# Performance work log

Measured on AMD Instinct MI355X. Metric: run time of the kernel, lower is better.

Reference implementation:

```python
import math
import jax, jax.numpy as jnp
import numpy as np

HEAD_DIM = 128
NUM_HEADS = 16
NUM_KV_HEADS = 4
CAUSAL = True


def rotate_half(x):
    x1 = x[..., : x.shape[-1] // 2]
    x2 = x[..., x.shape[-1] // 2 :]
    return jnp.concatenate([-x2, x1], axis=-1)


def setup_inputs() -> dict:
    key = jax.random.key(0)
    k1, k2, k3, k4, k5 = jax.random.split(key, 5)
    B, S, H = 2, 2048, 2048
    total_heads = NUM_HEADS + 2 * NUM_KV_HEADS  # 24
    hidden_states = jax.random.normal(k1, (B, S, H), dtype=jnp.float32)
    cos = jax.random.normal(k2, (S, HEAD_DIM), dtype=jnp.float32)
    sin = jax.random.normal(k3, (S, HEAD_DIM), dtype=jnp.float32)
    # eqx.nn.Linear weight layout: [out_features, in_features], y = W @ x
    w_qkv = jax.random.normal(k4, (total_heads * HEAD_DIM, H), dtype=jnp.float32) / math.sqrt(H)
    w_o = jax.random.normal(k5, (H, NUM_HEADS * HEAD_DIM), dtype=jnp.float32) / math.sqrt(NUM_HEADS * HEAD_DIM)
    return {"hidden_states": hidden_states, "cos": cos, "sin": sin, "w_qkv": w_qkv, "w_o": w_o}


def reference(hidden_states, cos, sin, w_qkv, w_o):
    B, S, _ = hidden_states.shape
    # fused QKV projection: [B,S,total_heads,head_dim]
    qkv = jnp.einsum("bsh,oh->bso", hidden_states, w_qkv).reshape(B, S, -1, HEAD_DIM)
    q = qkv[:, :, :NUM_HEADS]
    k = qkv[:, :, NUM_HEADS : NUM_HEADS + NUM_KV_HEADS]
    v = qkv[:, :, NUM_HEADS + NUM_KV_HEADS :]
    # RoPE: cos/sin [S,head_dim] -> broadcast [S,1,head_dim] over heads
    c = cos[..., None, :]
    s_ = sin[..., None, :]
    q = q * c + rotate_half(q) * s_
    k = k * c + rotate_half(k) * s_
    # GQA: repeat K/V across query-head groups
    rep = NUM_HEADS // NUM_KV_HEADS
    k = jnp.repeat(k, rep, axis=2)
    v = jnp.repeat(v, rep, axis=2)
    scale = 1.0 / math.sqrt(HEAD_DIM)
    scores = jnp.einsum("bshd,bthd->bhst", q, k) * scale  # [B,H,S,S]
    if CAUSAL:
        mask = jnp.tril(jnp.ones((S, S), dtype=bool))[None, None]
        scores = jnp.where(mask, scores, jnp.float32(-1e10))
    attn = jax.nn.softmax(scores, axis=-1)
    out = jnp.einsum("bhst,bthd->bshd", attn, v).reshape(B, S, -1)
    return jnp.einsum("bsd,od->bso", out, w_o)
```

## Files before the change

kernel.cpp:

```cpp
#include <hip/hip_runtime.h>
#include <hip/hip_bf16.h>
#include <stdint.h>

typedef __hip_bfloat16 bf16;
typedef __attribute__((ext_vector_type(8))) __bf16 bf16x8;
typedef __attribute__((ext_vector_type(4))) float f32x4;
typedef __attribute__((ext_vector_type(16))) float f32x16;
typedef __attribute__((ext_vector_type(4))) unsigned int u32x4;

#define QSCALE_LOG2E (0.08838834764831845f * 1.4426950408889634f)

__device__ __forceinline__ float fast_exp2(float x) {
#if __has_builtin(__builtin_amdgcn_exp2f)
  return __builtin_amdgcn_exp2f(x);
#else
  return exp2f(x);
#endif
}

__device__ __forceinline__ void gload_lds16(const void* g, void* l) {
  __builtin_amdgcn_global_load_lds(
      (__attribute__((address_space(1))) void*)(uintptr_t)g,
      (__attribute__((address_space(3))) void*)(uint32_t)(uintptr_t)l,
      16, 0, 0);
}

__global__ void cast_f32_to_bf16(const float* __restrict__ in,
                                 bf16* __restrict__ out, int n) {
  const int n4 = n >> 2;
  const int stride = gridDim.x * blockDim.x;
  for (int i = blockIdx.x * blockDim.x + threadIdx.x; i < n4; i += stride) {
    float4 v = reinterpret_cast<const float4*>(in)[i];
    bf16 tmp[4];
    tmp[0] = __float2bfloat16(v.x);
    tmp[1] = __float2bfloat16(v.y);
    tmp[2] = __float2bfloat16(v.z);
    tmp[3] = __float2bfloat16(v.w);
    reinterpret_cast<uint2*>(out)[i] = *reinterpret_cast<uint2*>(tmp);
  }
}

__device__ __forceinline__ void store_c(float v, bf16* p) { *p = __float2bfloat16(v); }
__device__ __forceinline__ void store_c(float v, float* p) { *p = v; }

__device__ __forceinline__ bf16x8 rd_swz(const bf16* base, int row, int ks, int hi) {
  const int byte = row * 128 + ((ks * 64 + hi * 16) ^ ((row & 7) << 4));
  return *reinterpret_cast<const bf16x8*>((const char*)base + byte);
}

__device__ __forceinline__ void stage_part(const bf16* __restrict__ g, int K,
                                           int kt, bf16* ldsBase, int part,
                                           int tid) {
  const int ga = part * 512 + tid;
  const int r = ga >> 3;
  const int gl = ga & 7;
  const int col = kt * 64 + ((gl ^ (r & 7)) << 3);
  gload_lds16(g + (size_t)r * K + col, (char*)ldsBase + ga * 16);
}

#define DS_A(QR)                                                              \
  _Pragma("unroll") for (int m = 0; m < 4; ++m)                               \
  _Pragma("unroll") for (int ks = 0; ks < 2; ++ks)                            \
      af[m][ks] = rd_swz(Acur, wm * 128 + (QR) * 64 + m * 16 + lr, ks, hi);

#define DS_B0()                                                               \
  _Pragma("unroll") for (int n = 0; n < NQ0; ++n)                             \
  _Pragma("unroll") for (int ks = 0; ks < 2; ++ks)                            \
      bf0[n][ks] = rd_swz(Bcur, wn * WN + n * 16 + lr, ks, hi);

#define DS_B1()                                                               \
  _Pragma("unroll") for (int n = 0; n < NQ1; ++n)                             \
  _Pragma("unroll") for (int ks = 0; ks < 2; ++ks)                            \
      bf1[n][ks] = rd_swz(Bcur, wn * WN + (NQ0 + n) * 16 + lr, ks, hi);

#define MFMA_Q0(QR)                                                           \
  __builtin_amdgcn_s_setprio(1);                                             \
  _Pragma("unroll") for (int ks = 0; ks < 2; ++ks)                            \
  _Pragma("unroll") for (int m = 0; m < 4; ++m)                               \
  _Pragma("unroll") for (int n = 0; n < NQ0; ++n)                             \
      acc[(QR) * 4 + m][n] = __builtin_amdgcn_mfma_f32_16x16x32_bf16(         \
          af[m][ks], bf0[n][ks], acc[(QR) * 4 + m][n], 0, 0, 0);              \
  __builtin_amdgcn_s_setprio(0);

#define MFMA_Q1(QR)                                                           \
  __builtin_amdgcn_s_setprio(1);                                             \
  _Pragma("unroll") for (int ks = 0; ks < 2; ++ks)                            \
  _Pragma("unroll") for (int m = 0; m < 4; ++m)                               \
  _Pragma("unroll") for (int n = 0; n < NQ1; ++n)                             \
      acc[(QR) * 4 + m][NQ0 + n] = __builtin_amdgcn_mfma_f32_16x16x32_bf16(   \
          af[m][ks], bf1[n][ks], acc[(QR) * 4 + m][NQ0 + n], 0, 0, 0);        \
  __builtin_amdgcn_s_setprio(0);

#define PHASE_SYNC_PRE()                                \
  __builtin_amdgcn_s_barrier();                         \
  asm volatile("s_waitcnt lgkmcnt(0)" ::: "memory");    \
  __builtin_amdgcn_sched_barrier(0);

#define PHASE_END() __builtin_amdgcn_s_barrier();

#define VMCNT_LB()                                                            \
  if constexpr (LB == 2) asm volatile("s_waitcnt vmcnt(2)" ::: "memory");     \
  else if constexpr (LB == 3) asm volatile("s_waitcnt vmcnt(3)" ::: "memory");\
  else asm volatile("s_waitcnt vmcnt(4)" ::: "memory");

template <int BN, typename OutT>
__global__ __launch_bounds__(512, 2) void gemm256(const bf16* __restrict__ A,
                                                  const bf16* __restrict__ B,
                                                  OutT* __restrict__ C,
                                                  int M, int N, int K, int NBX) {
  constexpr int NFRAG = BN / 64;
  constexpr int NQ0 = (NFRAG + 1) / 2;
  constexpr int NQ1 = NFRAG - NQ0;
  constexpr int WN = BN / 4;
  constexpr int LB = BN / 64;
  constexpr int LB0 = (LB + 1) / 2;
  constexpr int LB1 = LB - LB0;

  extern __shared__ bf16 sm[];
  bf16* A0 = sm;
  bf16* A1 = sm + 16384;
  bf16* B0 = sm + 32768;
  bf16* B1 = B0 + BN * 64;

  const int tid = threadIdx.x;
  const int lane = tid & 63;
  const int w = tid >> 6;
  const int wm = w >> 2;
  const int wn = w & 3;
  const int lr = lane & 15;
  const int hi = lane >> 4;

  const int nwg = gridDim.x;
  const int cpx = nwg >> 3;
  const int bid = blockIdx.x;
  const int wg = (bid & 7) * cpx + (bid >> 3);
  const int bx = wg % NBX;
  const int by = wg / NBX;
  const int row0 = by * 256;
  const int col0 = bx * BN;

  const bf16* Ag = A + (size_t)row0 * K;
  const bf16* Bg = B + (size_t)col0 * K;

#pragma unroll
  for (int p = 0; p < 4; ++p) stage_part(Ag, K, 0, A0, p, tid);
#pragma unroll
  for (int p = 0; p < LB; ++p) stage_part(Bg, K, 0, B0, p, tid);
#pragma unroll
  for (int p = 0; p < LB; ++p) stage_part(Bg, K, 1, B1, p, tid);
  VMCNT_LB();
  __builtin_amdgcn_s_barrier();

  f32x4 acc[8][NFRAG] = {};
  bf16x8 af[4][2], bf0[NQ0][2], bf1[NQ1 ? NQ1 : 1][2];

  const int iters = K >> 7;
  for (int i = 0; i < iters; ++i) {
    const bool g2 = (i + 1 < iters);
    const int t1 = 2 * i + 1, t2 = 2 * i + 2, t3 = 2 * i + 3;
    {
      const bf16* Acur = A0;
      const bf16* Bcur = B0;
      DS_A(0); DS_B0();
      stage_part(Ag, K, t1, A1, 0, tid);
      stage_part(Ag, K, t1, A1, 1, tid);
      PHASE_SYNC_PRE(); MFMA_Q0(0); PHASE_END();
      DS_B1();
      stage_part(Ag, K, t1, A1, 2, tid);
      stage_part(Ag, K, t1, A1, 3, tid);
      PHASE_SYNC_PRE(); MFMA_Q1(0); PHASE_END();
      DS_A(1);
      if (g2) {
#pragma unroll
        for (int p = 0; p < LB0; ++p) stage_part(Bg, K, t2, B0, p, tid);
      }
      PHASE_SYNC_PRE(); MFMA_Q0(1); PHASE_END();
      if (g2) {
#pragma unroll
        for (int p = 0; p < LB1; ++p) stage_part(Bg, K, t2, B0, LB0 + p, tid);
        VMCNT_LB();
      } else {
        asm volatile("s_waitcnt vmcnt(0)" ::: "memory");
      }
      PHASE_SYNC_PRE(); MFMA_Q1(1); PHASE_END();
    }
    {
      const bf16* Acur = A1;
      const bf16* Bcur = B1;
      DS_A(0); DS_B0();
      if (g2) {
        stage_part(Ag, K, t2, A0, 0, tid);
        stage_part(Ag, K, t2, A0, 1, tid);
      }
      PHASE_SYNC_PRE(); MFMA_Q0(0); PHASE_END();
      DS_B1();
      if (g2) {
        stage_part(Ag, K, t2, A0, 2, tid);
        stage_part(Ag, K, t2, A0, 3, tid);
      }
      PHASE_SYNC_PRE(); MFMA_Q1(0); PHASE_END();
      DS_A(1);
      if (g2) {
#pragma unroll
        for (int p = 0; p < LB0; ++p) stage_part(Bg, K, t3, B1, p, tid);
      }
      PHASE_SYNC_PRE(); MFMA_Q0(1); PHASE_END();
      if (g2) {
#pragma unroll
        for (int p = 0; p < LB1; ++p) stage_part(Bg, K, t3, B1, LB0 + p, tid);
        VMCNT_LB();
      } else {
        asm volatile("s_waitcnt vmcnt(0)" ::: "memory");
      }
      PHASE_SYNC_PRE(); MFMA_Q1(1); PHASE_END();
    }
  }

#pragma unroll
  for (int mi = 0; mi < 8; ++mi)
#pragma unroll
    for (int ni = 0; ni < NFRAG; ++ni)
#pragma unroll
      for (int j = 0; j < 4; ++j) {
        const int r = row0 + wm * 128 + mi * 16 + hi * 4 + j;
        const int cc = col0 + wn * WN + ni * 16 + lr;
        store_c(acc[mi][ni][j], &C[(size_t)r * N + cc]);
      }
}

__global__ void rope_scatter(const bf16* __restrict__ qkv,
                             const float* __restrict__ cs,
                             const float* __restrict__ sn,
                             bf16* __restrict__ Q, bf16* __restrict__ Kd) {
  const int tok = blockIdx.x;
  const int b = tok >> 11;
  const int s = tok & 2047;
  const bf16* row = qkv + (size_t)tok * 3072;
  for (int idx = threadIdx.x; idx < 1280; idx += blockDim.x) {
    const int head = idx >> 6;
    const int j = idx & 63;
    float x1 = __bfloat162float(row[head * 128 + j]);
    float x2 = __bfloat162float(row[head * 128 + j + 64]);
    const float c1 = cs[s * 128 + j];
    const float c2 = cs[s * 128 + j + 64];
    const float s1 = sn[s * 128 + j];
    const float s2 = sn[s * 128 + j + 64];
    float y1 = x1 * c1 - x2 * s1;
    float y2 = x2 * c2 + x1 * s2;
    bf16* dst;
    if (head < 16) {
      y1 *= QSCALE_LOG2E;
      y2 *= QSCALE_LOG2E;
      dst = Q + ((size_t)(b * 16 + head) * 2048 + s) * 128;
    } else {
      dst = Kd + ((size_t)(b * 4 + head - 16) * 2048 + s) * 128;
    }
    dst[j] = __float2bfloat16(y1);
    dst[j + 64] = __float2bfloat16(y2);
  }
}

__global__ __launch_bounds__(256) void vtrans(const bf16* __restrict__ qkv,
                                              bf16* __restrict__ Vt) {
  __shared__ bf16 tile[64 * 136];
  const int bid = blockIdx.x;
  const int stile = bid & 31;
  const int hv = (bid >> 5) & 3;
  const int b = bid >> 7;
  const int tid = threadIdx.x;
  const int tok0 = stile * 64;
  const bf16* src = qkv + (size_t)(b * 2048 + tok0) * 3072 + 2560 + hv * 128;
#pragma unroll
  for (int i = 0; i < 4; ++i) {
    const int c = tid + i * 256;
    const int r = c >> 4;
    const int off = (c & 15) * 8;
    uint4 d = *reinterpret_cast<const uint4*>(src + (size_t)r * 3072 + off);
    *reinterpret_cast<uint4*>(&tile[r * 136 + off]) = d;
  }
  __syncthreads();
  bf16* dst = Vt + ((size_t)(b * 4 + hv) * 128) * 2048 + tok0;
#pragma unroll
  for (int i = 0; i < 4; ++i) {
    const int o = tid + i * 256;
    const int d = o >> 3;
    const int s0 = (o & 7) * 8;
    bf16 vals[8];
#pragma unroll
    for (int j = 0; j < 8; ++j) vals[j] = tile[(s0 + j) * 136 + d];
    *reinterpret_cast<uint4*>(dst + (size_t)d * 2048 + s0) =
        *reinterpret_cast<const uint4*>(vals);
  }
}

__device__ __forceinline__ void stage_k(const bf16* __restrict__ Kb, int k0,
                                        bf16* dst, int w, int lane) {
#pragma unroll
  for (int i = 0; i < 4; ++i) {
    const int L16 = i * 256 + w * 64 + lane;
    const int row = L16 >> 4;
    const int colb = (L16 & 15) * 16;
    const int src = colb ^ ((row & 7) << 4);
    gload_lds16(Kb + (size_t)(k0 + row) * 128 + (src >> 1),
                (char*)dst + (i * 256 + w * 64) * 16);
  }
}

__device__ __forceinline__ void stage_v(const bf16* __restrict__ Vtb, int k0,
                                        bf16* dst, int w, int lane) {
#pragma unroll
  for (int i = 0; i < 4; ++i) {
    const int L16 = i * 256 + w * 64 + lane;
    const int row = L16 >> 3;
    const int colb = (L16 & 7) * 16;
    const int src = colb ^ ((row & 7) << 4);
    gload_lds16(Vtb + (size_t)row * 2048 + k0 + (src >> 1),
                (char*)dst + (i * 256 + w * 64) * 16);
  }
}

__device__ __forceinline__ bf16x8 lds_read_swz(const bf16* base, int row,
                                               int colElem, int rowBytes) {
  const int byte = row * rowBytes + (((colElem * 2) ^ ((row & 7) << 4)));
  return *reinterpret_cast<const bf16x8*>((const char*)base + byte);
}

__global__ __launch_bounds__(256, 2) void attn_fwd(const bf16* __restrict__ Qg,
                                                   const bf16* __restrict__ Kg,
                                                   const bf16* __restrict__ Vtg,
                                                   bf16* __restrict__ Og) {
  __shared__ bf16 Ks[2][64 * 128];
  __shared__ bf16 Vs[2][128 * 64];

  const int tid = threadIdx.x;
  const int lane = tid & 63;
  const int w = tid >> 6;
  const int bid = blockIdx.x;
  int qt, bh;
  if (bid < 256) { qt = bid & 15; bh = bid >> 4; }
  else           { qt = 15 - (bid & 15); bh = 16 + ((bid - 256) >> 4); }
  const int b = bh >> 4;
  const int h = bh & 15;
  const int kvh = h >> 2;
  const int q31 = lane & 31;
  const int hw = lane >> 5;

  const bf16* Qb = Qg + ((size_t)(b * 16 + h) * 2048) * 128;
  const bf16* Kb = Kg + ((size_t)(b * 4 + kvh) * 2048) * 128;
  const bf16* Vtb = Vtg + ((size_t)(b * 4 + kvh) * 128) * 2048;

  const int qw = qt * 128 + w * 32;

  bf16x8 qf[8];
#pragma unroll
  for (int db = 0; db < 8; ++db)
    qf[db] = *reinterpret_cast<const bf16x8*>(Qb + (size_t)(qw + q31) * 128 +
                                              db * 16 + hw * 8);

  f32x16 acc[4] = {};
  float mrow = -1e30f;
  float lsum = 0.f;

  const int nt = 2 * qt + 2;

  stage_k(Kb, 0, &Ks[0][0], w, lane);
  stage_v(Vtb, 0, &Vs[0][0], w, lane);

  for (int t = 0; t < nt; ++t) {
    const int cur = t & 1;
    if (t + 1 < nt) {
      stage_k(Kb, (t + 1) * 64, &Ks[cur ^ 1][0], w, lane);
      stage_v(Vtb, (t + 1) * 64, &Vs[cur ^ 1][0], w, lane);
      asm volatile("s_waitcnt vmcnt(8)" ::: "memory");
    } else {
      asm volatile("s_waitcnt vmcnt(0)" ::: "memory");
    }
    __builtin_amdgcn_s_barrier();
    __builtin_amdgcn_sched_barrier(0);

    const int k0 = t * 64;
    const bool active = (k0 <= qw + 31);
    if (active) {
      const bf16* Kt = &Ks[cur][0];
      const bf16* Vtl = &Vs[cur][0];

      f32x16 sacc[2] = {};
#pragma unroll
      for (int kb = 0; kb < 2; ++kb)
#pragma unroll
        for (int db = 0; db < 8; ++db) {
          bf16x8 kf = lds_read_swz(Kt, kb * 32 + q31, db * 16 + hw * 8, 256);
          sacc[kb] = __builtin_amdgcn_mfma_f32_32x32x16_bf16(kf, qf[db],
                                                             sacc[kb], 0, 0, 0);
        }

      float p[2][16];
#pragma unroll
      for (int kb = 0; kb < 2; ++kb)
#pragma unroll
        for (int r = 0; r < 16; ++r) p[kb][r] = sacc[kb][r];

      if (k0 + 63 > qw) {
        const int qg = qw + q31;
#pragma unroll
        for (int kb = 0; kb < 2; ++kb)
#pragma unroll
          for (int r = 0; r < 16; ++r) {
            const int k = k0 + kb * 32 + (r & 3) + 8 * (r >> 2) + 4 * hw;
            if (k > qg) p[kb][r] = -1e30f;
          }
      }

      float mt = p[0][0];
#pragma unroll
      for (int r = 1; r < 16; ++r) mt = fmaxf(mt, p[0][r]);
#pragma unroll
      for (int r = 0; r < 16; ++r) mt = fmaxf(mt, p[1][r]);
      mt = fmaxf(mt, __shfl_xor(mt, 32));

      if (__any(mt > mrow + 11.5f)) {
        const float mnew = fmaxf(mrow, mt);
        const float alpha = fast_exp2(mrow - mnew);
        mrow = mnew;
        lsum *= alpha;
        float areg[16];
#pragma unroll
        for (int r = 0; r < 16; ++r) {
          const int qloc = (r & 3) + 8 * (r >> 2) + 4 * hw;
          areg[r] = __shfl(alpha, qloc + (lane & 32));
        }
#pragma unroll
        for (int db = 0; db < 4; ++db)
#pragma unroll
          for (int r = 0; r < 16; ++r) acc[db][r] *= areg[r];
      }

      float rs = 0.f;
#pragma unroll
      for (int kb = 0; kb < 2; ++kb)
#pragma unroll
        for (int r = 0; r < 16; ++r) {
          const float pe = fast_exp2(p[kb][r] - mrow);
          p[kb][r] = pe;
          rs += pe;
        }
      rs += __shfl_xor(rs, 32);
      lsum += rs;

      unsigned int pk[2][8];
#pragma unroll
      for (int kb = 0; kb < 2; ++kb)
#pragma unroll
        for (int i = 0; i < 8; ++i)
          asm("v_cvt_pk_bf16_f32 %0, %1, %2"
              : "=v"(pk[kb][i])
              : "v"(p[kb][2 * i]), "v"(p[kb][2 * i + 1]));

#pragma unroll
      for (int kb16 = 0; kb16 < 4; ++kb16) {
        const int kb = kb16 >> 1;
        const int j0 = (kb16 & 1) * 4;
        unsigned int a0 = pk[kb][j0 + 0], b0 = pk[kb][j0 + 2];
        unsigned int a1 = pk[kb][j0 + 1], b1 = pk[kb][j0 + 3];
        asm volatile("v_permlane32_swap_b32 %0, %1" : "+v"(a0), "+v"(b0));
        asm volatile("v_permlane32_swap_b32 %0, %1" : "+v"(a1), "+v"(b1));
        u32x4 afu;
        afu.x = a0; afu.y = a1; afu.z = b0; afu.w = b1;
        bf16x8 pa;
        __builtin_memcpy(&pa, &afu, 16);
#pragma unroll
        for (int db = 0; db < 4; ++db) {
          bf16x8 vf = lds_read_swz(Vtl, db * 32 + q31, kb16 * 16 + hw * 8, 128);
          acc[db] = __builtin_amdgcn_mfma_f32_32x32x16_bf16(pa, vf,
                                                            acc[db], 0, 0, 0);
        }
      }
    }

    __builtin_amdgcn_sched_barrier(0);
    __builtin_amdgcn_s_barrier();
  }

  const float inv = 1.0f / lsum;
  float invq[16];
#pragma unroll
  for (int r = 0; r < 16; ++r) {
    const int qloc = (r & 3) + 8 * (r >> 2) + 4 * hw;
    invq[r] = __shfl(inv, qloc + (lane & 32));
  }
#pragma unroll
  for (int db = 0; db < 4; ++db)
#pragma unroll
    for (int r = 0; r < 16; ++r) {
      const int qg = qw + (r & 3) + 8 * (r >> 2) + 4 * hw;
      const int dg = db * 32 + q31;
      Og[((size_t)(b * 2048 + qg)) * 2048 + h * 128 + dg] =
          __float2bfloat16(acc[db][r] * invq[r]);
    }
}

extern "C" void kernel_launch(void* const* d_in, const int* in_sizes, int n_in,
                              void* d_out, int out_size, void* d_ws,
                              size_t ws_size, hipStream_t stream) {
  const float* hidden = (const float*)d_in[0];
  const float* cs = (const float*)d_in[1];
  const float* sn = (const float*)d_in[2];
  const float* wqkv = (const float*)d_in[3];
  const float* wo = (const float*)d_in[4];
  float* out = (float*)d_out;

  bf16* p = (bf16*)d_ws;
  bf16* hid_b = p;   p += 8388608;
  bf16* wqkv_b = p;  p += 6291456;
  bf16* wo_b = p;    p += 4194304;
  bf16* qkv = p;     p += 12582912;
  bf16* Qs = p;      p += 8388608;
  bf16* Ksc = p;     p += 2097152;
  bf16* Vt = p;      p += 2097152;

  (void)hipFuncSetAttribute((const void*)gemm256<192, bf16>,
                            hipFuncAttributeMaxDynamicSharedMemorySize, 131072);
  (void)hipFuncSetAttribute((const void*)gemm256<128, float>,
                            hipFuncAttributeMaxDynamicSharedMemorySize, 131072);

  cast_f32_to_bf16<<<2048, 256, 0, stream>>>(hidden, hid_b, 8388608);
  cast_f32_to_bf16<<<1536, 256, 0, stream>>>(wqkv, wqkv_b, 6291456);
  cast_f32_to_bf16<<<1024, 256, 0, stream>>>(wo, wo_b, 4194304);

  gemm256<192, bf16><<<256, 512, 114688, stream>>>(hid_b, wqkv_b, qkv,
                                                   4096, 3072, 2048, 16);
  rope_scatter<<<4096, 256, 0, stream>>>(qkv, cs, sn, Qs, Ksc);
  vtrans<<<256, 256, 0, stream>>>(qkv, Vt);

  bf16* aout = hid_b;
  attn_fwd<<<512, 256, 0, stream>>>(Qs, Ksc, Vt, aout);

  gemm256<128, float><<<256, 512, 98304, stream>>>(aout, wo_b, out,
                                                   4096, 2048, 2048, 16);
}
```

Before: 176.7 us.

## Replace LDS-staged K/V tiles with per-wave direct global register loads

Removes the shared-memory double buffer and block barriers from the attention loop. Each wave now loads its own 32-key K and V fragments directly from global memory into registers, prefetching the next tile after the MFMAs that consume the current one. Each wave also stops at its own causal bound instead of the block's, so no wave idles through inactive tiles. In exchange, each wave re-reads K/V from global memory or L2 without sharing across the four waves, and there is less latency hiding because only one tile is prefetched in registers.

Result: slower. 240.4 us (+36.1%).

```diff
diff --git a/kernel.cpp b/kernel.cpp
--- a/kernel.cpp
+++ b/kernel.cpp
@@ -293,45 +293,10 @@
   }
 }
 
-__device__ __forceinline__ void stage_k(const bf16* __restrict__ Kb, int k0,
-                                        bf16* dst, int w, int lane) {
-#pragma unroll
-  for (int i = 0; i < 4; ++i) {
-    const int L16 = i * 256 + w * 64 + lane;
-    const int row = L16 >> 4;
-    const int colb = (L16 & 15) * 16;
-    const int src = colb ^ ((row & 7) << 4);
-    gload_lds16(Kb + (size_t)(k0 + row) * 128 + (src >> 1),
-                (char*)dst + (i * 256 + w * 64) * 16);
-  }
-}
-
-__device__ __forceinline__ void stage_v(const bf16* __restrict__ Vtb, int k0,
-                                        bf16* dst, int w, int lane) {
-#pragma unroll
-  for (int i = 0; i < 4; ++i) {
-    const int L16 = i * 256 + w * 64 + lane;
-    const int row = L16 >> 3;
-    const int colb = (L16 & 7) * 16;
-    const int src = colb ^ ((row & 7) << 4);
-    gload_lds16(Vtb + (size_t)row * 2048 + k0 + (src >> 1),
-                (char*)dst + (i * 256 + w * 64) * 16);
-  }
-}
-
-__device__ __forceinline__ bf16x8 lds_read_swz(const bf16* base, int row,
-                                               int colElem, int rowBytes) {
-  const int byte = row * rowBytes + (((colElem * 2) ^ ((row & 7) << 4)));
-  return *reinterpret_cast<const bf16x8*>((const char*)base + byte);
-}
-
 __global__ __launch_bounds__(256, 2) void attn_fwd(const bf16* __restrict__ Qg,
                                                    const bf16* __restrict__ Kg,
                                                    const bf16* __restrict__ Vtg,
                                                    bf16* __restrict__ Og) {
-  __shared__ bf16 Ks[2][64 * 128];
-  __shared__ bf16 Vs[2][128 * 64];
-
   const int tid = threadIdx.x;
   const int lane = tid & 63;
   const int w = tid >> 6;
@@ -361,124 +326,116 @@
   float mrow = -1e30f;
   float lsum = 0.f;
 
-  const int nt = 2 * qt + 2;
-
-  stage_k(Kb, 0, &Ks[0][0], w, lane);
-  stage_v(Vtb, 0, &Vs[0][0], w, lane);
-
-  for (int t = 0; t < nt; ++t) {
-    const int cur = t & 1;
-    if (t + 1 < nt) {
-      stage_k(Kb, (t + 1) * 64, &Ks[cur ^ 1][0], w, lane);
-      stage_v(Vtb, (t + 1) * 64, &Vs[cur ^ 1][0], w, lane);
-      asm volatile("s_waitcnt vmcnt(8)" ::: "memory");
-    } else {
-      asm volatile("s_waitcnt vmcnt(0)" ::: "memory");
-    }
-    __builtin_amdgcn_s_barrier();
-    __builtin_amdgcn_sched_barrier(0);
-
-    const int k0 = t * 64;
-    const bool active = (k0 <= qw + 31);
-    if (active) {
-      const bf16* Kt = &Ks[cur][0];
-      const bf16* Vtl = &Vs[cur][0];
-
-      f32x16 sacc[2] = {};
-#pragma unroll
-      for (int kb = 0; kb < 2; ++kb)
-#pragma unroll
-        for (int db = 0; db < 8; ++db) {
-          bf16x8 kf = lds_read_swz(Kt, kb * 32 + q31, db * 16 + hw * 8, 256);
-          sacc[kb] = __builtin_amdgcn_mfma_f32_32x32x16_bf16(kf, qf[db],
-                                                             sacc[kb], 0, 0, 0);
-        }
-
-      float p[2][16];
-#pragma unroll
-      for (int kb = 0; kb < 2; ++kb)
-#pragma unroll
-        for (int r = 0; r < 16; ++r) p[kb][r] = sacc[kb][r];
-
-      if (k0 + 63 > qw) {
-        const int qg = qw + q31;
-#pragma unroll
-        for (int kb = 0; kb < 2; ++kb)
-#pragma unroll
-          for (int r = 0; r < 16; ++r) {
-            const int k = k0 + kb * 32 + (r & 3) + 8 * (r >> 2) + 4 * hw;
-            if (k > qg) p[kb][r] = -1e30f;
-          }
-      }
-
-      float mt = p[0][0];
-#pragma unroll
-      for (int r = 1; r < 16; ++r) mt = fmaxf(mt, p[0][r]);
-#pragma unroll
-      for (int r = 0; r < 16; ++r) mt = fmaxf(mt, p[1][r]);
-      mt = fmaxf(mt, __shfl_xor(mt, 32));
-
-      if (__any(mt > mrow + 11.5f)) {
-        const float mnew = fmaxf(mrow, mt);
-        const float alpha = fast_exp2(mrow - mnew);
-        mrow = mnew;
-        lsum *= alpha;
-        float areg[16];
-#pragma unroll
-        for (int r = 0; r < 16; ++r) {
-          const int qloc = (r & 3) + 8 * (r >> 2) + 4 * hw;
-          areg[r] = __shfl(alpha, qloc + (lane & 32));
-        }
-#pragma unroll
-        for (int db = 0; db < 4; ++db)
-#pragma unroll
-          for (int r = 0; r < 16; ++r) acc[db][r] *= areg[r];
-      }
-
-      float rs = 0.f;
-#pragma unroll
-      for (int kb = 0; kb < 2; ++kb)
-#pragma unroll
-        for (int r = 0; r < 16; ++r) {
-          const float pe = fast_exp2(p[kb][r] - mrow);
-          p[kb][r] = pe;
-          rs += pe;
-        }
-      rs += __shfl_xor(rs, 32);
-      lsum += rs;
-
-      unsigned int pk[2][8];
-#pragma unroll
-      for (int kb = 0; kb < 2; ++kb)
-#pragma unroll
-        for (int i = 0; i < 8; ++i)
-          asm("v_cvt_pk_bf16_f32 %0, %1, %2"
-              : "=v"(pk[kb][i])
-              : "v"(p[kb][2 * i]), "v"(p[kb][2 * i + 1]));
-
-#pragma unroll
-      for (int kb16 = 0; kb16 < 4; ++kb16) {
-        const int kb = kb16 >> 1;
-        const int j0 = (kb16 & 1) * 4;
-        unsigned int a0 = pk[kb][j0 + 0], b0 = pk[kb][j0 + 2];
-        unsigned int a1 = pk[kb][j0 + 1], b1 = pk[kb][j0 + 3];
-        asm volatile("v_permlane32_swap_b32 %0, %1" : "+v"(a0), "+v"(b0));
-        asm volatile("v_permlane32_swap_b32 %0, %1" : "+v"(a1), "+v"(b1));
-        u32x4 afu;
-        afu.x = a0; afu.y = a1; afu.z = b0; afu.w = b1;
-        bf16x8 pa;
-        __builtin_memcpy(&pa, &afu, 16);
-#pragma unroll
-        for (int db = 0; db < 4; ++db) {
-          bf16x8 vf = lds_read_swz(Vtl, db * 32 + q31, kb16 * 16 + hw * 8, 128);
-          acc[db] = __builtin_amdgcn_mfma_f32_32x32x16_bf16(pa, vf,
-                                                            acc[db], 0, 0, 0);
-        }
-      }
-    }
-
-    __builtin_amdgcn_sched_barrier(0);
-    __builtin_amdgcn_s_barrier();
+  const int ntw = (qw >> 5) + 1;
+
+  const bf16* kbase = Kb + (size_t)q31 * 128 + hw * 8;
+  const bf16* vbase = Vtb + (size_t)q31 * 2048 + hw * 8;
+
+  bf16x8 kreg[8], vreg[8];
+#pragma unroll
+  for (int db = 0; db < 8; ++db)
+    kreg[db] = *reinterpret_cast<const bf16x8*>(kbase + db * 16);
+#pragma unroll
+  for (int i = 0; i < 8; ++i) {
+    const int kb16 = i >> 2, db = i & 3;
+    vreg[i] = *reinterpret_cast<const bf16x8*>(vbase + (size_t)(db * 32) * 2048 +
+                                               kb16 * 16);
+  }
+
+  for (int t = 0; t < ntw; ++t) {
+    const int k0 = t * 32;
+
+    f32x16 sacc = {};
+#pragma unroll
+    for (int db = 0; db < 8; ++db)
+      sacc = __builtin_amdgcn_mfma_f32_32x32x16_bf16(kreg[db], qf[db], sacc,
+                                                     0, 0, 0);
+
+    if (t + 1 < ntw) {
+      const bf16* kb2 = kbase + (size_t)(k0 + 32) * 128;
+#pragma unroll
+      for (int db = 0; db < 8; ++db)
+        kreg[db] = *reinterpret_cast<const bf16x8*>(kb2 + db * 16);
+    }
+
+    float p[16];
+#pragma unroll
+    for (int r = 0; r < 16; ++r) p[r] = sacc[r];
+
+    if (t == ntw - 1) {
+      const int qg = qw + q31;
+#pragma unroll
+      for (int r = 0; r < 16; ++r) {
+        const int k = k0 + (r & 3) + 8 * (r >> 2) + 4 * hw;
+        if (k > qg) p[r] = -1e30f;
+      }
+    }
+
+    float mt = p[0];
+#pragma unroll
+    for (int r = 1; r < 16; ++r) mt = fmaxf(mt, p[r]);
+    mt = fmaxf(mt, __shfl_xor(mt, 32));
+
+    if (__any(mt > mrow + 11.5f)) {
+      const float mnew = fmaxf(mrow, mt);
+      const float alpha = fast_exp2(mrow - mnew);
+      mrow = mnew;
+      lsum *= alpha;
+      float areg[16];
+#pragma unroll
+      for (int r = 0; r < 16; ++r) {
+        const int qloc = (r & 3) + 8 * (r >> 2) + 4 * hw;
+        areg[r] = __shfl(alpha, qloc + (lane & 32));
+      }
+#pragma unroll
+      for (int db = 0; db < 4; ++db)
+#pragma unroll
+        for (int r = 0; r < 16; ++r) acc[db][r] *= areg[r];
+    }
+
+    float rs = 0.f;
+#pragma unroll
+    for (int r = 0; r < 16; ++r) {
+      const float pe = fast_exp2(p[r] - mrow);
+      p[r] = pe;
+      rs += pe;
+    }
+    rs += __shfl_xor(rs, 32);
+    lsum += rs;
+
+    unsigned int pk[8];
+#pragma unroll
+    for (int i = 0; i < 8; ++i)
+      asm("v_cvt_pk_bf16_f32 %0, %1, %2"
+          : "=v"(pk[i])
+          : "v"(p[2 * i]), "v"(p[2 * i + 1]));
+
+#pragma unroll
+    for (int kb16 = 0; kb16 < 2; ++kb16) {
+      const int j0 = kb16 * 4;
+      unsigned int a0 = pk[j0 + 0], b0 = pk[j0 + 2];
+      unsigned int a1 = pk[j0 + 1], b1 = pk[j0 + 3];
+      asm volatile("v_permlane32_swap_b32 %0, %1" : "+v"(a0), "+v"(b0));
+      asm volatile("v_permlane32_swap_b32 %0, %1" : "+v"(a1), "+v"(b1));
+      u32x4 afu;
+      afu.x = a0; afu.y = a1; afu.z = b0; afu.w = b1;
+      bf16x8 pa;
+      __builtin_memcpy(&pa, &afu, 16);
+#pragma unroll
+      for (int db = 0; db < 4; ++db)
+        acc[db] = __builtin_amdgcn_mfma_f32_32x32x16_bf16(
+            pa, vreg[kb16 * 4 + db], acc[db], 0, 0, 0);
+    }
+
+    if (t + 1 < ntw) {
+      const bf16* vb2 = vbase + (k0 + 32);
+#pragma unroll
+      for (int i = 0; i < 8; ++i) {
+        const int kb16 = i >> 2, db = i & 3;
+        vreg[i] = *reinterpret_cast<const bf16x8*>(
+            vb2 + (size_t)(db * 32) * 2048 + kb16 * 16);
+      }
+    }
   }
 
   const float inv = 1.0f / lsum;
```
